# Performance work log

Measured on AMD Instinct MI355X. Metric: run time of the kernel, lower is better.

Reference implementation:

```python
import jax, jax.numpy as jnp
import numpy as np

EPS = 1e-6

def normalize(a):
    # L1 row-normalization over the last dim (works for [b,f,n,n] and [b,n,n])
    return a / (jnp.sum(jnp.abs(a), axis=-1, keepdims=True) + EPS)

def setup_inputs() -> dict:
    key = jax.random.key(0)
    ks = jax.random.split(key, 10)
    B, NC, F_, NE, R = 32, 62, 256, 512, 16
    s = 0.05
    return {
        "x": jax.random.normal(ks[0], (B, NC, F_), dtype=jnp.float32),
        "p": jax.random.normal(ks[1], (NC, NC), dtype=jnp.float32) * s,
        "bias": jnp.zeros((NC, F_), dtype=jnp.float32),
        "q_mat": jax.random.normal(ks[2], (F_, F_), dtype=jnp.float32) * s,
        "theta": jax.random.normal(ks[3], (F_, NC * F_), dtype=jnp.float32) * s,
        "codebook": jax.random.normal(ks[4], (NE, F_), dtype=jnp.float32) * s,
        "se_w1": jax.random.normal(ks[5], (F_, F_ // R), dtype=jnp.float32) * s,
        "se_b1": jnp.zeros((F_ // R,), dtype=jnp.float32),
        "se_w2": jax.random.normal(ks[6], (F_ // R, F_), dtype=jnp.float32) * s,
        "se_b2": jnp.zeros((F_,), dtype=jnp.float32),
    }

def reference(x, p, bias, q_mat, theta, codebook, se_w1, se_b1, se_w2, se_b2):
    elu = jax.nn.elu
    commitment = 0.25
    # o = p @ x + bias : [b, nc, f]
    o = jnp.einsum('ij,bjd->bid', p, x) + bias
    # g = ELU(o @ q @ theta) : [b, nc, nc*f]
    g = elu((o @ q_mat) @ theta)
    b, nc = g.shape[0], g.shape[1]
    adj = g.reshape(b, nc, nc, -1).transpose(0, 3, 1, 2)  # [b, f, nc, nc]
    adj = normalize(adj)
    # ---- VQ codebook quantization ----
    d = codebook.shape[1]
    z = adj.transpose(0, 2, 3, 1).reshape(-1, d)  # [b*nc*nc, d]
    dist = (jnp.sum(z * z, axis=-1, keepdims=True)
            - 2.0 * z @ codebook.T
            + jnp.sum(codebook * codebook, axis=-1))  # [N, num_embedding]
    idx = jnp.argmin(dist, axis=-1)
    zq = codebook[idx]
    e_loss = jnp.mean((jax.lax.stop_gradient(zq) - z) ** 2)
    q_loss = jnp.mean((zq - jax.lax.stop_gradient(z)) ** 2)
    vq_loss = q_loss + commitment * e_loss
    zq_st = z + jax.lax.stop_gradient(zq - z)  # straight-through
    counts = jnp.zeros((codebook.shape[0],), dtype=z.dtype).at[idx].add(1.0)
    probs = counts / idx.shape[0]
    usage = jnp.exp(-jnp.sum(probs * jnp.log(probs + 1e-10)))  # perplexity
    adj_recon = zq_st.reshape(b, nc, nc, d).transpose(0, 3, 1, 2)  # [b, f, nc, nc]
    # ---- SE block + residual ----
    s = jnp.mean(adj_recon, axis=(2, 3))  # squeeze: [b, f]
    s = jax.nn.sigmoid(jax.nn.relu(s @ se_w1 + se_b1) @ se_w2 + se_b2)
    adj_recon = elu(adj_recon * s[:, :, None, None] + adj_recon)
    # reduce over feature channels, ELU, normalize : [b, nc, nc]
    adj_recon = normalize(elu(jnp.sum(adj_recon, axis=1)))
    return (vq_loss, adj_recon, usage, codebook)
```

## Files before the change

### kernel.cpp

```cpp
#include <hip/hip_runtime.h>
#include <math.h>

#define B_   32
#define NCq  62
#define F_   256
#define NE   512
#define M_   (B_*NCq)
#define NCOL (NCq*F_)
#define NZ   (M_*NCq)
#define EPSF 1e-6f

typedef unsigned short ushort_t;
typedef unsigned int uint_t;
typedef _Float16 h8_t __attribute__((ext_vector_type(8)));
typedef float f4_t __attribute__((ext_vector_type(4)));

__device__ __forceinline__ float eluf(float x){ return x > 0.0f ? x : expm1f(x); }

__device__ __forceinline__ int sw_off(int row, int piece){
    return row*32 + ((piece ^ ((row>>1)&3))*8);
}
__device__ __forceinline__ void gl_lds(const _Float16* g, _Float16* l){
    __builtin_amdgcn_global_load_lds((const __attribute__((address_space(1))) void*)g,
                                     (__attribute__((address_space(3))) void*)l, 16, 0, 0);
}

__global__ __launch_bounds__(256) void k_split_th(const float* __restrict__ TH,
                                                  _Float16* __restrict__ THf){
    __shared__ float tile[32][33];
    int n0 = blockIdx.x * 32, k0 = blockIdx.y * 32;
    int tid = threadIdx.x;
    int cc = tid & 31, rr = tid >> 5;
    #pragma unroll
    for(int p=0;p<4;p++){
        int kk = rr + p*8;
        tile[kk][cc] = TH[(size_t)(k0+kk)*NCOL + n0 + cc];
    }
    __syncthreads();
    #pragma unroll
    for(int p=0;p<4;p++){
        int nn = rr + p*8;
        THf[(size_t)(n0+nn)*F_ + k0 + cc] = (_Float16)tile[cc][nn];
    }
}

__global__ __launch_bounds__(256) void k_prep(const float* __restrict__ cb,
                                              _Float16* __restrict__ CBf,
                                              float* __restrict__ cnorm, float* __restrict__ out_cb){
    int e = blockIdx.x; int d = threadIdx.x;
    float v = cb[e*F_ + d];
    out_cb[e*F_ + d] = v;
    CBf[e*F_ + d] = (_Float16)v;
    float s = v*v;
    #pragma unroll
    for(int m=32;m;m>>=1) s += __shfl_xor(s, m, 64);
    __shared__ float red[4];
    if((threadIdx.x & 63)==0) red[threadIdx.x>>6] = s;
    __syncthreads();
    if(threadIdx.x==0) cnorm[e] = red[0]+red[1]+red[2]+red[3];
}

__global__ __launch_bounds__(256) void k_ot(const float* __restrict__ x, const float* __restrict__ p,
                                            const float* __restrict__ bias, const float* __restrict__ q,
                                            _Float16* __restrict__ Thh, _Float16* __restrict__ Thl){
    int bi = blockIdx.x; int d = threadIdx.x;
    int b = bi / NCq, i = bi % NCq;
    __shared__ float pr[NCq];
    __shared__ float orow[F_];
    if(d < NCq) pr[d] = p[i*NCq + d];
    __syncthreads();
    float acc = bias[i*F_ + d];
    const float* xb = x + (size_t)b*NCq*F_ + d;
    #pragma unroll 2
    for(int j=0;j<NCq;j++) acc = fmaf(pr[j], xb[j*F_], acc);
    orow[d] = acc;
    __syncthreads();
    float t = 0.f;
    #pragma unroll 4
    for(int k=0;k<F_;k++) t = fmaf(orow[k], q[k*F_ + d], t);
    _Float16 h = (_Float16)t;
    Thh[bi*F_ + d] = h;
    Thl[bi*F_ + d] = (_Float16)(t - (float)h);
}

__global__ __launch_bounds__(256,2) void k_gemm_g(const _Float16* __restrict__ Thh, const _Float16* __restrict__ Thl,
                                                  const _Float16* __restrict__ THf,
                                                  _Float16* __restrict__ Gf){
    __shared__ _Float16 Ahh[128*32], Ahl[128*32], Bs[256*32];
    int tid = threadIdx.x;
    int l = tid & 63, w = tid >> 6;
    int wr = w >> 1, wc = w & 1;
    int m = l & 15, quad = l >> 4;
    int row0 = blockIdx.x * 128, col0 = blockIdx.y * 256;
    int wbase = tid & 192;
    f4_t acc[4][8] = {};
    for(int kc=0; kc<F_; kc+=32){
        #pragma unroll
        for(int p2=0;p2<2;p2++){
            int idx = p2*256 + tid;
            int row = idx >> 2, psw = idx & 3;
            int porig = psw ^ ((row>>1)&3);
            int rclamp = row0 + row; if(rclamp >= M_) rclamp = M_-1;
            size_t go = (size_t)rclamp*F_ + kc + porig*8;
            gl_lds(&Thh[go], &Ahh[(p2*256 + wbase)*8]);
            gl_lds(&Thl[go], &Ahl[(p2*256 + wbase)*8]);
        }
        #pragma unroll
        for(int p2=0;p2<4;p2++){
            int idx = p2*256 + tid;
            int row = idx >> 2, psw = idx & 3;
            int porig = psw ^ ((row>>1)&3);
            size_t go = (size_t)(col0 + row)*F_ + kc + porig*8;
            gl_lds(&THf[go], &Bs[(p2*256 + wbase)*8]);
        }
        __syncthreads();
        h8_t a_h[4], a_l[4];
        #pragma unroll
        for(int mt=0;mt<4;mt++){
            int row = wr*64 + mt*16 + m;
            int off = sw_off(row, quad);
            a_h[mt] = *(const h8_t*)&Ahh[off];
            a_l[mt] = *(const h8_t*)&Ahl[off];
        }
        #pragma unroll
        for(int nt=0;nt<8;nt++){
            int col = wc*128 + nt*16 + m;
            int off = sw_off(col, quad);
            h8_t b = *(const h8_t*)&Bs[off];
            #pragma unroll
            for(int mt=0;mt<4;mt++){
                acc[mt][nt] = __builtin_amdgcn_mfma_f32_16x16x32_f16(a_h[mt], b, acc[mt][nt], 0,0,0);
                acc[mt][nt] = __builtin_amdgcn_mfma_f32_16x16x32_f16(a_l[mt], b, acc[mt][nt], 0,0,0);
            }
        }
        __syncthreads();
    }
    #pragma unroll
    for(int mt=0;mt<4;mt++){
        #pragma unroll
        for(int nt=0;nt<8;nt++){
            int rowb = row0 + wr*64 + mt*16 + quad*4;
            int colb = col0 + wc*128 + nt*16 + m;
            #pragma unroll
            for(int r=0;r<4;r++){
                int row = rowb + r;
                if(row < M_) Gf[(size_t)row*NCOL + colb] = (_Float16)eluf(acc[mt][nt][r]);
            }
        }
    }
}

__global__ __launch_bounds__(256) void k_den(_Float16* __restrict__ Gf, double* __restrict__ loss_sum){
    int bi = blockIdx.x;
    int tid = threadIdx.x;
    int dg = tid & 31, jg = tid >> 5;
    __shared__ float l1[8][32][8];
    __shared__ float l2[8][32][8];
    __shared__ float invsh[32][8];
    float v[8][8];
    float a1[8] = {}, a2[8] = {};
    size_t base = (size_t)bi*NCOL + dg*8;
    #pragma unroll
    for(int p=0;p<8;p++){
        int j = jg + p*8;
        if(j < NCq){
            h8_t g = *(const h8_t*)&Gf[base + (size_t)j*F_];
            #pragma unroll
            for(int i=0;i<8;i++){
                float t = (float)g[i];
                v[p][i] = t;
                a1[i] += fabsf(t);
                a2[i] = fmaf(t, t, a2[i]);
            }
        }
    }
    #pragma unroll
    for(int i=0;i<8;i++){ l1[jg][dg][i] = a1[i]; l2[jg][dg][i] = a2[i]; }
    __syncthreads();
    if(jg == 0){
        float part = 0.f;
        #pragma unroll
        for(int i=0;i<8;i++){
            float s1 = 0.f, s2 = 0.f;
            #pragma unroll
            for(int q2=0;q2<8;q2++){ s1 += l1[q2][dg][i]; s2 += l2[q2][dg][i]; }
            float inv = 1.0f/(s1 + EPSF);
            invsh[dg][i] = inv;
            part += s2*inv*inv;
        }
        #pragma unroll
        for(int mk=16;mk;mk>>=1) part += __shfl_xor(part, mk, 32);
        if(tid == 0) atomicAdd(loss_sum, (double)part);
    }
    __syncthreads();
    float inv[8];
    #pragma unroll
    for(int i=0;i<8;i++) inv[i] = invsh[dg][i];
    #pragma unroll
    for(int p=0;p<8;p++){
        int j = jg + p*8;
        if(j < NCq){
            h8_t z;
            #pragma unroll
            for(int i=0;i<8;i++) z[i] = (_Float16)(v[p][i]*inv[i]);
            *(h8_t*)&Gf[base + (size_t)j*F_] = z;
        }
    }
}

__global__ __launch_bounds__(256,2) void k_vq(const _Float16* __restrict__ Zf,
                                              const _Float16* __restrict__ CBf,
                                              const float* __restrict__ cnorm,
                                              float* __restrict__ pmin, int* __restrict__ pidx){
    __shared__ _Float16 As[128*32], Bs[256*32];
    int tid = threadIdx.x;
    int l = tid & 63, w = tid >> 6;
    int wr = w >> 1, wc = w & 1;
    int m = l & 15, quad = l >> 4;
    int n_base = blockIdx.x * 128;
    int e0 = blockIdx.y * 256;
    int wbase = tid & 192;
    f4_t acc[4][8] = {};
    for(int kc=0; kc<F_; kc+=32){
        #pragma unroll
        for(int p2=0;p2<2;p2++){
            int idx = p2*256 + tid;
            int row = idx >> 2, psw = idx & 3;
            int porig = psw ^ ((row>>1)&3);
            size_t go = (size_t)(n_base + row)*F_ + kc + porig*8;
            gl_lds(&Zf[go], &As[(p2*256 + wbase)*8]);
        }
        #pragma unroll
        for(int p2=0;p2<4;p2++){
            int idx = p2*256 + tid;
            int row = idx >> 2, psw = idx & 3;
            int porig = psw ^ ((row>>1)&3);
            size_t go = (size_t)(e0 + row)*F_ + kc + porig*8;
            gl_lds(&CBf[go], &Bs[(p2*256 + wbase)*8]);
        }
        __syncthreads();
        h8_t a[4];
        #pragma unroll
        for(int mt=0;mt<4;mt++){
            int row = wr*64 + mt*16 + m;
            a[mt] = *(const h8_t*)&As[sw_off(row, quad)];
        }
        #pragma unroll
        for(int nt=0;nt<8;nt++){
            int col = wc*128 + nt*16 + m;
            h8_t b = *(const h8_t*)&Bs[sw_off(col, quad)];
            #pragma unroll
            for(int mt=0;mt<4;mt++)
                acc[mt][nt] = __builtin_amdgcn_mfma_f32_16x16x32_f16(a[mt], b, acc[mt][nt], 0,0,0);
        }
        __syncthreads();
    }
    #pragma unroll
    for(int mt=0;mt<4;mt++){
        float bv[4]; int bix[4];
        #pragma unroll
        for(int r=0;r<4;r++){ bv[r] = 3.4e38f; bix[r] = 0; }
        #pragma unroll
        for(int nt=0;nt<8;nt++){
            int e = e0 + wc*128 + nt*16 + m;
            float cn = cnorm[e];
            #pragma unroll
            for(int r=0;r<4;r++){
                float vv = cn - 2.0f*acc[mt][nt][r];
                if(vv < bv[r]){ bv[r] = vv; bix[r] = e; }
            }
        }
        #pragma unroll
        for(int r=0;r<4;r++){
            float vv = bv[r]; int ix = bix[r];
            #pragma unroll
            for(int mk=8;mk;mk>>=1){
                float ov = __shfl_xor(vv, mk, 64);
                int   oi = __shfl_xor(ix, mk, 64);
                if(ov < vv || (ov == vv && oi < ix)){ vv = ov; ix = oi; }
            }
            if(m == 0){
                int n = n_base + wr*64 + mt*16 + quad*4 + r;
                int slot = blockIdx.y*2 + wc;
                pmin[n*4 + slot] = vv;
                pidx[n*4 + slot] = ix;
            }
        }
    }
}

__global__ __launch_bounds__(1024) void k_fin(const float* __restrict__ pmin, const int* __restrict__ pidx,
                                              int* __restrict__ idx,
                                              int* __restrict__ counts, int* __restrict__ countb,
                                              double* __restrict__ loss_sum){
    int b = blockIdx.x;
    int t = threadIdx.x;
    __shared__ int hist[NE];
    __shared__ float red[16];
    #pragma unroll
    for(int e=t; e<NE; e+=1024) hist[e] = 0;
    __syncthreads();
    float msum = 0.f;
    int n0 = b * (NCq*NCq);
    for(int i=t; i<NCq*NCq; i+=1024){
        int n = n0 + i;
        float4 pv = *(const float4*)&pmin[n*4];
        int4   pi = *(const int4*)&pidx[n*4];
        float bv = pv.x; int bix = pi.x;
        if(pv.y < bv || (pv.y==bv && pi.y<bix)){ bv=pv.y; bix=pi.y; }
        if(pv.z < bv || (pv.z==bv && pi.z<bix)){ bv=pv.z; bix=pi.z; }
        if(pv.w < bv || (pv.w==bv && pi.w<bix)){ bv=pv.w; bix=pi.w; }
        idx[n] = bix;
        atomicAdd(&hist[bix], 1);
        msum += bv;
    }
    #pragma unroll
    for(int m=32;m;m>>=1) msum += __shfl_xor(msum, m, 64);
    if((t&63)==0) red[t>>6] = msum;
    __syncthreads();
    if(t==0){
        float s = 0.f;
        #pragma unroll
        for(int i2=0;i2<16;i2++) s += red[i2];
        atomicAdd(loss_sum, (double)s);
    }
    for(int e=t; e<NE; e+=1024){
        int c = hist[e];
        countb[b*NE + e] = c;
        if(c) atomicAdd(&counts[e], c);
    }
}

__global__ __launch_bounds__(256) void k_scal(const int* __restrict__ counts, const double* __restrict__ loss_sum,
                                              float* __restrict__ out){
    int t = threadIdx.x;
    float ent = 0.f;
    for(int e=t; e<NE; e+=256){
        float pr = (float)counts[e] / (float)NZ;
        ent += pr * logf(pr + 1e-10f);
    }
    #pragma unroll
    for(int m=32;m;m>>=1) ent += __shfl_xor(ent,m,64);
    __shared__ float red[4];
    if((t&63)==0) red[t>>6]=ent;
    __syncthreads();
    if(t==0){
        float e2 = red[0]+red[1]+red[2]+red[3];
        out[1+NZ] = expf(-e2);
        out[0] = (float)(1.25 * (*loss_sum) / ((double)NZ * (double)F_));
    }
}

__global__ __launch_bounds__(256) void k_se(const int* __restrict__ countb, const float* __restrict__ cb,
                                            const float* __restrict__ w1, const float* __restrict__ b1,
                                            const float* __restrict__ w2, const float* __restrict__ b2,
                                            float* __restrict__ s2p1){
    int b = blockIdx.x; int d = threadIdx.x;
    __shared__ float cnt[NE];
    __shared__ float s_sh[F_];
    __shared__ float h_sh[16];
    cnt[d]       = (float)countb[b*NE + d];
    cnt[d + 256] = (float)countb[b*NE + d + 256];
    __syncthreads();
    float s = 0.f;
    for(int e=0;e<NE;e++) s = fmaf(cnt[e], cb[e*F_ + d], s);
    s *= (1.0f/(float)(NCq*NCq));
    s_sh[d] = s;
    __syncthreads();
    if(d < 16){
        float h = b1[d];
        for(int k=0;k<F_;k++) h = fmaf(s_sh[k], w1[k*16 + d], h);
        h_sh[d] = fmaxf(h, 0.f);
    }
    __syncthreads();
    float v = b2[d];
    #pragma unroll
    for(int r=0;r<16;r++) v = fmaf(h_sh[r], w2[r*F_ + d], v);
    s2p1[b*F_ + d] = 1.0f + 1.0f/(1.0f + expf(-v));
}

__global__ __launch_bounds__(256) void k_w(const float* __restrict__ cb, const float* __restrict__ s2p1,
                                           float* __restrict__ wtab){
    int b = blockIdx.x; int eg = blockIdx.y;
    int wv = threadIdx.x>>6, lane = threadIdx.x&63;
    __shared__ float m_sh[F_];
    m_sh[threadIdx.x] = s2p1[b*F_ + threadIdx.x];
    __syncthreads();
    int e = eg*4 + wv;
    float4 c4 = *(const float4*)&cb[e*F_ + lane*4];
    float s = eluf(c4.x*m_sh[lane*4]) + eluf(c4.y*m_sh[lane*4+1])
            + eluf(c4.z*m_sh[lane*4+2]) + eluf(c4.w*m_sh[lane*4+3]);
    #pragma unroll
    for(int m2=32;m2;m2>>=1) s += __shfl_xor(s,m2,64);
    if(lane==0) wtab[b*NE + e] = s;
}

__global__ __launch_bounds__(64) void k_out(const int* __restrict__ idx, const float* __restrict__ wtab,
                                            float* __restrict__ out){
    int bi = blockIdx.x; int j = threadIdx.x;
    int b = bi / NCq;
    float v = 0.f;
    if(j < NCq) v = eluf(wtab[b*NE + idx[bi*NCq + j]]);
    float a = fabsf(v);
    #pragma unroll
    for(int m=32;m;m>>=1) a += __shfl_xor(a,m,64);
    if(j < NCq) out[1 + bi*NCq + j] = v / (a + EPSF);
}

extern "C" void kernel_launch(void* const* d_in, const int* in_sizes, int n_in,
                              void* d_out, int out_size, void* d_ws, size_t ws_size,
                              hipStream_t stream){
    (void)in_sizes; (void)n_in; (void)out_size; (void)ws_size;
    const float* x    = (const float*)d_in[0];
    const float* p    = (const float*)d_in[1];
    const float* bias = (const float*)d_in[2];
    const float* q    = (const float*)d_in[3];
    const float* th   = (const float*)d_in[4];
    const float* cb   = (const float*)d_in[5];
    const float* w1   = (const float*)d_in[6];
    const float* b1   = (const float*)d_in[7];
    const float* w2   = (const float*)d_in[8];
    const float* b2   = (const float*)d_in[9];
    float* out = (float*)d_out;
    char* ws = (char*)d_ws;
    size_t off = 0;
    auto alloc = [&](size_t bytes){ void* ptr = ws + off; off = (off + bytes + 255) & ~255ull; return ptr; };
    _Float16* Gf   = (_Float16*)alloc((size_t)NZ*F_*sizeof(_Float16));
    _Float16* THf  = (_Float16*)alloc((size_t)F_*NCOL*sizeof(_Float16));
    _Float16* Thh  = (_Float16*)alloc((size_t)M_*F_*sizeof(_Float16));
    _Float16* Thl  = (_Float16*)alloc((size_t)M_*F_*sizeof(_Float16));
    _Float16* CBf  = (_Float16*)alloc((size_t)NE*F_*sizeof(_Float16));
    float*    CN   = (float*)   alloc((size_t)NE*sizeof(float));
    float*    PMIN = (float*)   alloc((size_t)NZ*4*sizeof(float));
    int*      PIDX = (int*)     alloc((size_t)NZ*4*sizeof(int));
    int*      IDX  = (int*)     alloc((size_t)NZ*sizeof(int));
    char*     zbase= (char*)    alloc(8 + NE*sizeof(int));
    double*   LOSS   = (double*)zbase;
    int*      COUNTS = (int*)(zbase + 8);
    int*      COUNTB = (int*)   alloc((size_t)B_*NE*sizeof(int));
    float*    S2P1 = (float*)alloc((size_t)B_*F_*sizeof(float));
    float*    WTAB = (float*)alloc((size_t)B_*NE*sizeof(float));

    (void)hipMemsetAsync(zbase, 0, 8 + NE*sizeof(int), stream);
    dim3 gth(NCOL/32, F_/32);
    k_split_th<<<gth, 256, 0, stream>>>(th, THf);
    k_prep<<<NE, 256, 0, stream>>>(cb, CBf, CN, out + 1 + NZ + 1);
    k_ot<<<M_, 256, 0, stream>>>(x, p, bias, q, Thh, Thl);
    dim3 g3((M_ + 127)/128, NCOL/256);
    k_gemm_g<<<g3, 256, 0, stream>>>(Thh, Thl, THf, Gf);
    k_den<<<M_, 256, 0, stream>>>(Gf, LOSS);
    dim3 g5(NZ/128, 2);
    k_vq<<<g5, 256, 0, stream>>>(Gf, CBf, CN, PMIN, PIDX);
    k_fin<<<B_, 1024, 0, stream>>>(PMIN, PIDX, IDX, COUNTS, COUNTB, LOSS);
    k_scal<<<1, 256, 0, stream>>>(COUNTS, LOSS, out);
    k_se<<<B_, 256, 0, stream>>>(COUNTB, cb, w1, b1, w2, b2, S2P1);
    dim3 g8(B_, NE/4);
    k_w<<<g8, 256, 0, stream>>>(cb, S2P1, WTAB);
    k_out<<<M_, 64, 0, stream>>>(IDX, WTAB, out);
}
```

Before: 317.8 us.

## Drop hi/lo fp16 split of A operand and widen GEMM K-tiles to 64

The first GEMM no longer splits the o@q intermediate into high and low fp16 halves, which halves its MFMA count and A-operand traffic. Both GEMM kernels (k_gemm_g and k_vq) now stage K chunks of 64 instead of 32 per barrier, using a new 8-way XOR swizzle, so there are half as many sync and load phases. The cost is lower precision in g, which could flip argmin codebook choices, plus higher LDS use per block (48KB), which may limit occupancy.

```diff
diff --git a/kernel.cpp b/kernel.cpp
--- a/kernel.cpp
+++ b/kernel.cpp
@@ -17,8 +17,8 @@
 
 __device__ __forceinline__ float eluf(float x){ return x > 0.0f ? x : expm1f(x); }
 
-__device__ __forceinline__ int sw_off(int row, int piece){
-    return row*32 + ((piece ^ ((row>>1)&3))*8);
+__device__ __forceinline__ int sw64(int row, int piece){
+    return row*64 + ((piece ^ (row&7))*8);
 }
 __device__ __forceinline__ void gl_lds(const _Float16* g, _Float16* l){
     __builtin_amdgcn_global_load_lds((const __attribute__((address_space(1))) void*)g,
@@ -62,7 +62,7 @@
 
 __global__ __launch_bounds__(256) void k_ot(const float* __restrict__ x, const float* __restrict__ p,
                                             const float* __restrict__ bias, const float* __restrict__ q,
-                                            _Float16* __restrict__ Thh, _Float16* __restrict__ Thl){
+                                            _Float16* __restrict__ Tf){
     int bi = blockIdx.x; int d = threadIdx.x;
     int b = bi / NCq, i = bi % NCq;
     __shared__ float pr[NCq];
@@ -78,15 +78,13 @@
     float t = 0.f;
     #pragma unroll 4
     for(int k=0;k<F_;k++) t = fmaf(orow[k], q[k*F_ + d], t);
-    _Float16 h = (_Float16)t;
-    Thh[bi*F_ + d] = h;
-    Thl[bi*F_ + d] = (_Float16)(t - (float)h);
-}
-
-__global__ __launch_bounds__(256,2) void k_gemm_g(const _Float16* __restrict__ Thh, const _Float16* __restrict__ Thl,
+    Tf[bi*F_ + d] = (_Float16)t;
+}
+
+__global__ __launch_bounds__(256,2) void k_gemm_g(const _Float16* __restrict__ Tf,
                                                   const _Float16* __restrict__ THf,
                                                   _Float16* __restrict__ Gf){
-    __shared__ _Float16 Ahh[128*32], Ahl[128*32], Bs[256*32];
+    __shared__ _Float16 As[128*64], Bs[256*64];
     int tid = threadIdx.x;
     int l = tid & 63, w = tid >> 6;
     int wr = w >> 1, wc = w & 1;
@@ -94,43 +92,38 @@
     int row0 = blockIdx.x * 128, col0 = blockIdx.y * 256;
     int wbase = tid & 192;
     f4_t acc[4][8] = {};
-    for(int kc=0; kc<F_; kc+=32){
-        #pragma unroll
-        for(int p2=0;p2<2;p2++){
-            int idx = p2*256 + tid;
-            int row = idx >> 2, psw = idx & 3;
-            int porig = psw ^ ((row>>1)&3);
-            int rclamp = row0 + row; if(rclamp >= M_) rclamp = M_-1;
-            size_t go = (size_t)rclamp*F_ + kc + porig*8;
-            gl_lds(&Thh[go], &Ahh[(p2*256 + wbase)*8]);
-            gl_lds(&Thl[go], &Ahl[(p2*256 + wbase)*8]);
-        }
+    for(int kc=0; kc<F_; kc+=64){
         #pragma unroll
         for(int p2=0;p2<4;p2++){
             int idx = p2*256 + tid;
-            int row = idx >> 2, psw = idx & 3;
-            int porig = psw ^ ((row>>1)&3);
-            size_t go = (size_t)(col0 + row)*F_ + kc + porig*8;
-            gl_lds(&THf[go], &Bs[(p2*256 + wbase)*8]);
+            int row = idx >> 3, psw = idx & 7;
+            int porig = psw ^ (row&7);
+            int rclamp = row0 + row; if(rclamp >= M_) rclamp = M_-1;
+            gl_lds(&Tf[(size_t)rclamp*F_ + kc + porig*8], &As[(p2*256 + wbase)*8]);
+        }
+        #pragma unroll
+        for(int p2=0;p2<8;p2++){
+            int idx = p2*256 + tid;
+            int row = idx >> 3, psw = idx & 7;
+            int porig = psw ^ (row&7);
+            gl_lds(&THf[(size_t)(col0 + row)*F_ + kc + porig*8], &Bs[(p2*256 + wbase)*8]);
         }
         __syncthreads();
-        h8_t a_h[4], a_l[4];
-        #pragma unroll
-        for(int mt=0;mt<4;mt++){
-            int row = wr*64 + mt*16 + m;
-            int off = sw_off(row, quad);
-            a_h[mt] = *(const h8_t*)&Ahh[off];
-            a_l[mt] = *(const h8_t*)&Ahl[off];
-        }
-        #pragma unroll
-        for(int nt=0;nt<8;nt++){
-            int col = wc*128 + nt*16 + m;
-            int off = sw_off(col, quad);
-            h8_t b = *(const h8_t*)&Bs[off];
+        #pragma unroll
+        for(int ks=0;ks<2;ks++){
+            h8_t a[4];
             #pragma unroll
             for(int mt=0;mt<4;mt++){
-                acc[mt][nt] = __builtin_amdgcn_mfma_f32_16x16x32_f16(a_h[mt], b, acc[mt][nt], 0,0,0);
-                acc[mt][nt] = __builtin_amdgcn_mfma_f32_16x16x32_f16(a_l[mt], b, acc[mt][nt], 0,0,0);
+                int row = wr*64 + mt*16 + m;
+                a[mt] = *(const h8_t*)&As[sw64(row, ks*4 + quad)];
+            }
+            #pragma unroll
+            for(int nt=0;nt<8;nt++){
+                int col = wc*128 + nt*16 + m;
+                h8_t b = *(const h8_t*)&Bs[sw64(col, ks*4 + quad)];
+                #pragma unroll
+                for(int mt=0;mt<4;mt++)
+                    acc[mt][nt] = __builtin_amdgcn_mfma_f32_16x16x32_f16(a[mt], b, acc[mt][nt], 0,0,0);
             }
         }
         __syncthreads();
@@ -212,7 +205,7 @@
                                               const _Float16* __restrict__ CBf,
                                               const float* __restrict__ cnorm,
                                               float* __restrict__ pmin, int* __restrict__ pidx){
-    __shared__ _Float16 As[128*32], Bs[256*32];
+    __shared__ _Float16 As[128*64], Bs[256*64];
     int tid = threadIdx.x;
     int l = tid & 63, w = tid >> 6;
     int wr = w >> 1, wc = w & 1;
@@ -221,37 +214,38 @@
     int e0 = blockIdx.y * 256;
     int wbase = tid & 192;
     f4_t acc[4][8] = {};
-    for(int kc=0; kc<F_; kc+=32){
-        #pragma unroll
-        for(int p2=0;p2<2;p2++){
-            int idx = p2*256 + tid;
-            int row = idx >> 2, psw = idx & 3;
-            int porig = psw ^ ((row>>1)&3);
-            size_t go = (size_t)(n_base + row)*F_ + kc + porig*8;
-            gl_lds(&Zf[go], &As[(p2*256 + wbase)*8]);
-        }
+    for(int kc=0; kc<F_; kc+=64){
         #pragma unroll
         for(int p2=0;p2<4;p2++){
             int idx = p2*256 + tid;
-            int row = idx >> 2, psw = idx & 3;
-            int porig = psw ^ ((row>>1)&3);
-            size_t go = (size_t)(e0 + row)*F_ + kc + porig*8;
-            gl_lds(&CBf[go], &Bs[(p2*256 + wbase)*8]);
+            int row = idx >> 3, psw = idx & 7;
+            int porig = psw ^ (row&7);
+            gl_lds(&Zf[(size_t)(n_base + row)*F_ + kc + porig*8], &As[(p2*256 + wbase)*8]);
+        }
+        #pragma unroll
+        for(int p2=0;p2<8;p2++){
+            int idx = p2*256 + tid;
+            int row = idx >> 3, psw = idx & 7;
+            int porig = psw ^ (row&7);
+            gl_lds(&CBf[(size_t)(e0 + row)*F_ + kc + porig*8], &Bs[(p2*256 + wbase)*8]);
         }
         __syncthreads();
-        h8_t a[4];
-        #pragma unroll
-        for(int mt=0;mt<4;mt++){
-            int row = wr*64 + mt*16 + m;
-            a[mt] = *(const h8_t*)&As[sw_off(row, quad)];
-        }
-        #pragma unroll
-        for(int nt=0;nt<8;nt++){
-            int col = wc*128 + nt*16 + m;
-            h8_t b = *(const h8_t*)&Bs[sw_off(col, quad)];
-            #pragma unroll
-            for(int mt=0;mt<4;mt++)
-                acc[mt][nt] = __builtin_amdgcn_mfma_f32_16x16x32_f16(a[mt], b, acc[mt][nt], 0,0,0);
+        #pragma unroll
+        for(int ks=0;ks<2;ks++){
+            h8_t a[4];
+            #pragma unroll
+            for(int mt=0;mt<4;mt++){
+                int row = wr*64 + mt*16 + m;
+                a[mt] = *(const h8_t*)&As[sw64(row, ks*4 + quad)];
+            }
+            #pragma unroll
+            for(int nt=0;nt<8;nt++){
+                int col = wc*128 + nt*16 + m;
+                h8_t b = *(const h8_t*)&Bs[sw64(col, ks*4 + quad)];
+                #pragma unroll
+                for(int mt=0;mt<4;mt++)
+                    acc[mt][nt] = __builtin_amdgcn_mfma_f32_16x16x32_f16(a[mt], b, acc[mt][nt], 0,0,0);
+            }
         }
         __syncthreads();
     }
@@ -427,8 +421,7 @@
     auto alloc = [&](size_t bytes){ void* ptr = ws + off; off = (off + bytes + 255) & ~255ull; return ptr; };
     _Float16* Gf   = (_Float16*)alloc((size_t)NZ*F_*sizeof(_Float16));
     _Float16* THf  = (_Float16*)alloc((size_t)F_*NCOL*sizeof(_Float16));
-    _Float16* Thh  = (_Float16*)alloc((size_t)M_*F_*sizeof(_Float16));
-    _Float16* Thl  = (_Float16*)alloc((size_t)M_*F_*sizeof(_Float16));
+    _Float16* Tf   = (_Float16*)alloc((size_t)M_*F_*sizeof(_Float16));
     _Float16* CBf  = (_Float16*)alloc((size_t)NE*F_*sizeof(_Float16));
     float*    CN   = (float*)   alloc((size_t)NE*sizeof(float));
     float*    PMIN = (float*)   alloc((size_t)NZ*4*sizeof(float));
@@ -445,9 +438,9 @@
     dim3 gth(NCOL/32, F_/32);
     k_split_th<<<gth, 256, 0, stream>>>(th, THf);
     k_prep<<<NE, 256, 0, stream>>>(cb, CBf, CN, out + 1 + NZ + 1);
-    k_ot<<<M_, 256, 0, stream>>>(x, p, bias, q, Thh, Thl);
+    k_ot<<<M_, 256, 0, stream>>>(x, p, bias, q, Tf);
     dim3 g3((M_ + 127)/128, NCOL/256);
-    k_gemm_g<<<g3, 256, 0, stream>>>(Thh, Thl, THf, Gf);
+    k_gemm_g<<<g3, 256, 0, stream>>>(Tf, THf, Gf);
     k_den<<<M_, 256, 0, stream>>>(Gf, LOSS);
     dim3 g5(NZ/128, 2);
     k_vq<<<g5, 256, 0, stream>>>(Gf, CBf, CN, PMIN, PIDX);
```

Measured after the change: 303.1 us. -4.6%, faster.
